# Optimization experiments

Measured on AMD Instinct MI355X. Metric: run time of the kernel, lower is better.

## Reference

```python
import jax, jax.numpy as jnp
import numpy as np

B, L, D, H = 8192, 32, 128, 8  # batch nodes, max neighbors, embed dim, heads


def setup_inputs() -> dict:
    key = jax.random.key(0)
    ks = jax.random.split(key, 16)
    s = 0.05  # weight init scale
    return {
        "node_embeds": jax.random.normal(ks[0], (B, D), jnp.float32),
        "neighbor_embeds": jax.random.normal(ks[1], (B, L, D), jnp.float32),
        "node_degrees": jax.random.randint(ks[2], (B,), 1, L + 1),
        # layer 0 (concatenate=True): query_heads 128->1024, value_proj 128->128
        "wq0": jax.random.normal(ks[3], (H * D, D), jnp.float32) * s,
        "bq0": jax.random.normal(ks[4], (H * D,), jnp.float32) * s,
        "wv0": jax.random.normal(ks[5], (D, D), jnp.float32) * s,
        "bv0": jax.random.normal(ks[6], (D,), jnp.float32) * s,
        "wp0": jax.random.normal(ks[7], (D, D), jnp.float32) * s,
        "bp0": jax.random.normal(ks[8], (D,), jnp.float32) * s,
        # layer 1 (last, concatenate=False): query_heads 128->1024, value_proj 128->1024
        "wq1": jax.random.normal(ks[9], (H * D, D), jnp.float32) * s,
        "bq1": jax.random.normal(ks[10], (H * D,), jnp.float32) * s,
        "wv1": jax.random.normal(ks[11], (H * D, D), jnp.float32) * s,
        "bv1": jax.random.normal(ks[12], (H * D,), jnp.float32) * s,
        "wp1": jax.random.normal(ks[13], (D, D), jnp.float32) * s,
        "bp1": jax.random.normal(ks[14], (D,), jnp.float32) * s,
    }


def _attn_layer(node, neigh, mask, wq, bq, wv, bv, wp, bp, concatenate):
    # neigh: [B, L, D] (already zero-masked); mask: [B, L] bool
    b, l, d = neigh.shape
    dk = d  # attnhead_size == query_size == D for use_dot=True
    v = neigh @ wv.T + bv                      # [B, L, H*dv]
    dv = v.shape[-1] // H
    v = v.reshape(b, l, H, dv).transpose(0, 2, 1, 3)   # [B, H, L, dv]
    q = (node @ wq.T + bq).reshape(b, H, dk)           # [B, H, dk]
    scores = jnp.einsum('bhd,bld->bhl', q, neigh) / jnp.sqrt(jnp.float32(dk))
    scores = jnp.where(mask[:, None, :], scores, jnp.float32(-1e9))
    p = jax.nn.softmax(scores, axis=-1)                # [B, H, L]
    av = jnp.einsum('bhl,bhld->bhd', p, v)             # [B, H, dv]
    av = av.reshape(b, H * dv) if concatenate else av.mean(axis=1)
    return node @ wp.T + bp + av


def reference(node_embeds, neighbor_embeds, node_degrees,
              wq0, bq0, wv0, bv0, wp0, bp0,
              wq1, bq1, wv1, bv1, wp1, bp1):
    mask = jnp.arange(L)[None, :] < node_degrees[:, None]          # [B, L]
    neigh = jnp.where(mask[:, :, None], neighbor_embeds, 0.0)
    x = _attn_layer(node_embeds, neigh, mask, wq0, bq0, wv0, bv0, wp0, bp0, True)
    x = jax.nn.relu(x)  # activation on all but last layer
    x = _attn_layer(x, neigh, mask, wq1, bq1, wv1, bv1, wp1, bp1, False)
    return x
```

## Files before the change

### kernel.cpp

```cpp
#include <hip/hip_runtime.h>

constexpr int Ln = 32, Dn = 128, Hn = 8;

using bf16x8 = __attribute__((ext_vector_type(8))) short;
using f32x4  = __attribute__((ext_vector_type(4))) float;

__device__ __forceinline__ unsigned short f2bf(float f) {
    union { float f; unsigned u; } v; v.f = f;
    unsigned r = v.u + 0x7FFFu + ((v.u >> 16) & 1u);
    return (unsigned short)(r >> 16);
}
__device__ __forceinline__ float bf2f(unsigned short s) {
    union { unsigned u; float f; } v; v.u = ((unsigned)s) << 16; return v.f;
}
__device__ __forceinline__ bf16x8 cvt8(float4 a, float4 b) {
    bf16x8 r;
    r[0] = (short)f2bf(a.x); r[1] = (short)f2bf(a.y);
    r[2] = (short)f2bf(a.z); r[3] = (short)f2bf(a.w);
    r[4] = (short)f2bf(b.x); r[5] = (short)f2bf(b.y);
    r[6] = (short)f2bf(b.z); r[7] = (short)f2bf(b.w);
    return r;
}

constexpr int    CVT_ITEMS = 442368 + 2304;
constexpr size_t WS_NEED   = 442368ull * 2 + 2304ull * 4;

__global__ void cvt_weights(const float* __restrict__ wq0, const float* __restrict__ bq0,
                            const float* __restrict__ wv0, const float* __restrict__ bv0,
                            const float* __restrict__ wp0, const float* __restrict__ bp0,
                            const float* __restrict__ wq1, const float* __restrict__ bq1,
                            const float* __restrict__ wv1, const float* __restrict__ bv1,
                            const float* __restrict__ wp1, const float* __restrict__ bp1,
                            unsigned short* __restrict__ ws)
{
    const float scale = 0.08838834764831845f;
    int tid = blockIdx.x * 256 + threadIdx.x;
    if (tid >= CVT_ITEMS) return;
    if (tid < 442368) {
        float v;
        if      (tid < 131072) v = wq0[tid] * scale;
        else if (tid < 262144) v = wq1[tid - 131072] * scale;
        else if (tid < 278528) v = wv0[tid - 262144];
        else if (tid < 294912) v = wp0[tid - 278528];
        else if (tid < 425984) v = wv1[tid - 294912] * 0.125f;
        else                   v = wp1[tid - 425984];
        ws[tid] = f2bf(v);
    } else {
        int j = tid - 442368;
        float* fws = (float*)(ws + 442368);
        if      (j < 1024) fws[j] = bq0[j] * scale;
        else if (j < 2048) fws[j] = bq1[j - 1024] * scale;
        else if (j < 2176) { int d = j - 2048; fws[j] = bp0[d] + bv0[d]; }
        else if (j < 2304) {
            int d = j - 2176;
            float s = 0.f;
            #pragma unroll
            for (int h = 0; h < Hn; ++h) s += bv1[h * Dn + d];
            fws[j] = bp1[d] + 0.125f * s;
        }
    }
}

__global__ __launch_bounds__(512, 4)
void gcn11(const float* __restrict__ nodeE, const float* __restrict__ neighE,
           const int* __restrict__ degp, const unsigned short* __restrict__ ws,
           float* __restrict__ out)
{
    __shared__ unsigned short sN[8][16][136];
    __shared__ unsigned short sQC[16 * 1096];
    __shared__ unsigned short sX[16][136];
    __shared__ float          sP[8][16][Hn];
    __shared__ float          sSum[8][Hn];
    __shared__ int            sDeg[16];

    const unsigned short* wq0b = ws;
    const unsigned short* wq1b = ws + 131072;
    const unsigned short* wv0b = ws + 262144;
    const unsigned short* wp0b = ws + 278528;
    const unsigned short* wv1b = ws + 294912;
    const unsigned short* wp1b = ws + 425984;
    const float* fws  = (const float*)(ws + 442368);
    const float* bq0s = fws;
    const float* bq1s = fws + 1024;
    const float* b0   = fws + 2048;
    const float* b1   = fws + 2176;

    const int t    = threadIdx.x;
    const int lane = t & 63;
    const int w    = t >> 6;
    const int row  = lane & 15;
    const int kg   = lane >> 4;
    const int node0 = blockIdx.x * 16;

    bf16x8 a[4];

    auto stage_half = [&](int node, int r0, int v) {
        const float* base = neighE + ((size_t)(node0 + node) * Ln + r0) * Dn;
        #pragma unroll
        for (int it = 0; it < 4; ++it) {
            int c = lane + 64 * it;
            int l = c >> 4, d8 = c & 15;
            if (l < v) {
                const float4* s = (const float4*)(base + (size_t)c * 8);
                *(bf16x8*)&sN[w][l][d8 * 8] = cvt8(s[0], s[1]);
            }
        }
    };

    auto qgemm = [&](const unsigned short* wqb, const float* bqs) {
        #pragma unroll
        for (int ks = 0; ks < 4; ++ks)
            a[ks] = *(const bf16x8*)&sX[row][ks * 32 + kg * 8];
        #pragma unroll
        for (int f = 0; f < 8; ++f) {
            int o = w * 128 + f * 16 + row;
            f32x4 acc = {0.f, 0.f, 0.f, 0.f};
            #pragma unroll
            for (int ks = 0; ks < 4; ++ks)
                acc = __builtin_amdgcn_mfma_f32_16x16x32_bf16(
                    a[ks], *(const bf16x8*)(wqb + (size_t)o * Dn + ks * 32 + kg * 8), acc, 0, 0, 0);
            float bias = bqs[o];
            #pragma unroll
            for (int rr = 0; rr < 4; ++rr)
                sQC[(kg * 4 + rr) * 1096 + w * 136 + f * 16 + row] = f2bf(acc[rr] + bias);
        }
    };

    auto pv_acc = [&](float (&c)[Hn][2], int v) {
        for (int l = 0; l < v; ++l) {
            unsigned nv = *(const unsigned*)&sN[w][l][2 * lane];
            float n0 = bf2f((unsigned short)(nv & 0xFFFFu));
            float n1 = bf2f((unsigned short)(nv >> 16));
            float4 p01 = *(const float4*)&sP[w][l][0];
            float4 p23 = *(const float4*)&sP[w][l][4];
            c[0][0] += p01.x * n0; c[0][1] += p01.x * n1;
            c[1][0] += p01.y * n0; c[1][1] += p01.y * n1;
            c[2][0] += p01.z * n0; c[2][1] += p01.z * n1;
            c[3][0] += p01.w * n0; c[3][1] += p01.w * n1;
            c[4][0] += p23.x * n0; c[4][1] += p23.x * n1;
            c[5][0] += p23.y * n0; c[5][1] += p23.y * n1;
            c[6][0] += p23.z * n0; c[6][1] += p23.z * n1;
            c[7][0] += p23.w * n0; c[7][1] += p23.w * n1;
        }
    };

    auto attn2 = [&](int node) {
        const int deg = sDeg[node];
        const int v0  = deg < 16 ? deg : 16;
        stage_half(node, 0, v0);

        const int hcol = row & 7;
        bf16x8 qf[4];
        #pragma unroll
        for (int ks = 0; ks < 4; ++ks)
            qf[ks] = *(const bf16x8*)&sQC[node * 1096 + hcol * 136 + ks * 32 + kg * 8];

        f32x4 s0 = {0.f,0.f,0.f,0.f};
        #pragma unroll
        for (int ks = 0; ks < 4; ++ks)
            s0 = __builtin_amdgcn_mfma_f32_16x16x32_bf16(
                *(const bf16x8*)&sN[w][row][ks * 32 + kg * 8], qf[ks], s0, 0, 0, 0);
        float sv[4];
        float sum = 0.f;
        #pragma unroll
        for (int j = 0; j < 4; ++j) {
            int l = kg * 4 + j;
            sv[j] = (l < v0) ? __expf(s0[j]) : 0.f;
            sum += sv[j];
        }
        sum += __shfl_xor(sum, 16);
        sum += __shfl_xor(sum, 32);
        if (row < 8) {
            #pragma unroll
            for (int j = 0; j < 4; ++j)
                sP[w][kg * 4 + j][row] = sv[j];
        }
        float c[Hn][2];
        #pragma unroll
        for (int h = 0; h < Hn; ++h) { c[h][0] = 0.f; c[h][1] = 0.f; }
        pv_acc(c, v0);

        if (deg > 16) {
            const int v1 = deg - 16;
            stage_half(node, 16, v1);
            f32x4 s1 = {0.f,0.f,0.f,0.f};
            #pragma unroll
            for (int ks = 0; ks < 4; ++ks)
                s1 = __builtin_amdgcn_mfma_f32_16x16x32_bf16(
                    *(const bf16x8*)&sN[w][row][ks * 32 + kg * 8], qf[ks], s1, 0, 0, 0);
            float sw[4];
            float sum1 = 0.f;
            #pragma unroll
            for (int j = 0; j < 4; ++j) {
                int l = kg * 4 + j;
                sw[j] = (l < v1) ? __expf(s1[j]) : 0.f;
                sum1 += sw[j];
            }
            sum1 += __shfl_xor(sum1, 16);
            sum1 += __shfl_xor(sum1, 32);
            sum += sum1;
            if (row < 8) {
                #pragma unroll
                for (int j = 0; j < 4; ++j)
                    sP[w][kg * 4 + j][row] = sw[j];
            }
            pv_acc(c, v1);
        }

        if (row < 8) sSum[w][row] = sum;
        float4 r01 = *(const float4*)&sSum[w][0];
        float4 r23 = *(const float4*)&sSum[w][4];
        float rh[Hn] = {r01.x, r01.y, r01.z, r01.w, r23.x, r23.y, r23.z, r23.w};
        #pragma unroll
        for (int h = 0; h < Hn; ++h) {
            float inv = 1.f / rh[h];
            unsigned pk = (unsigned)f2bf(c[h][0] * inv) | ((unsigned)f2bf(c[h][1] * inv) << 16);
            *(unsigned*)&sQC[node * 1096 + h * 136 + 2 * lane] = pk;
        }
    };

    if (t < 256) {
        int r = t >> 4, c = (t & 15) * 8;
        const float4* s = (const float4*)(nodeE + (size_t)(node0 + r) * Dn + c);
        *(bf16x8*)&sX[r][c] = cvt8(s[0], s[1]);
    }
    if (t < 16) sDeg[t] = degp[node0 + t];
    __syncthreads();

    qgemm(wq0b, bq0s);
    __syncthreads();

    attn2(w);
    attn2(8 + w);
    __syncthreads();

    {
        const int d = w * 16 + row;
        f32x4 pa = {0.f,0.f,0.f,0.f}, va = {0.f,0.f,0.f,0.f};
        #pragma unroll
        for (int ks = 0; ks < 4; ++ks) {
            pa = __builtin_amdgcn_mfma_f32_16x16x32_bf16(
                a[ks], *(const bf16x8*)(wp0b + (size_t)d * Dn + ks * 32 + kg * 8), pa, 0, 0, 0);
            bf16x8 c0 = *(const bf16x8*)&sQC[row * 1096 + w * 136 + ks * 32 + kg * 8];
            va = __builtin_amdgcn_mfma_f32_16x16x32_bf16(
                c0, *(const bf16x8*)(wv0b + (size_t)d * Dn + ks * 32 + kg * 8), va, 0, 0, 0);
        }
        float bias = b0[d];
        #pragma unroll
        for (int rr = 0; rr < 4; ++rr)
            sX[kg * 4 + rr][d] = f2bf(fmaxf(pa[rr] + va[rr] + bias, 0.f));
    }
    __syncthreads();

    qgemm(wq1b, bq1s);
    __syncthreads();

    attn2(w);
    attn2(8 + w);
    __syncthreads();

    {
        const int d = w * 16 + row;
        f32x4 pa = {0.f,0.f,0.f,0.f};
        #pragma unroll
        for (int ks = 0; ks < 4; ++ks)
            pa = __builtin_amdgcn_mfma_f32_16x16x32_bf16(
                a[ks], *(const bf16x8*)(wp1b + (size_t)d * Dn + ks * 32 + kg * 8), pa, 0, 0, 0);
        f32x4 g = {0.f,0.f,0.f,0.f};
        #pragma unroll 8
        for (int ks2 = 0; ks2 < 32; ++ks2) {
            int hk = ks2 * 32 + kg * 8;
            int h = hk >> 7, kk = hk & 127;
            bf16x8 c0 = *(const bf16x8*)&sQC[row * 1096 + h * 136 + kk];
            g = __builtin_amdgcn_mfma_f32_16x16x32_bf16(
                c0, *(const bf16x8*)(wv1b + ((size_t)(h * Dn + d)) * Dn + kk), g, 0, 0, 0);
        }
        float bias = b1[d];
        #pragma unroll
        for (int rr = 0; rr < 4; ++rr)
            out[(size_t)(node0 + kg * 4 + rr) * Dn + d] = pa[rr] + g[rr] + bias;
    }
}

__global__ __launch_bounds__(256, 2)
void gcn2(const float* __restrict__ nodeE, const float* __restrict__ neighE,
          const int* __restrict__ degp,
          const float* __restrict__ wq0, const float* __restrict__ bq0,
          const float* __restrict__ wv0, const float* __restrict__ bv0,
          const float* __restrict__ wp0, const float* __restrict__ bp0,
          const float* __restrict__ wq1, const float* __restrict__ bq1,
          const float* __restrict__ wv1, const float* __restrict__ bv1,
          const float* __restrict__ wp1, const float* __restrict__ bp1,
          float* __restrict__ out)
{
    __shared__ unsigned short sX[16][Dn];
    __shared__ unsigned short sQ[8][Hn][Dn];
    __shared__ unsigned short sN[4][Ln][Dn + 8];
    __shared__ float          sP[4][Hn][Ln];
    __shared__ unsigned short sC[8][Hn][Dn + 8];
    __shared__ int            sDeg[8];

    const int t    = threadIdx.x;
    const int lane = t & 63;
    const int w    = t >> 6;
    const int row  = lane & 15;
    const int kg   = lane >> 4;
    const int node0 = blockIdx.x * 8;
    const float scale = 0.08838834764831845f;

    {
        int i = t * 8, r = i >> 7, c = i & 127;
        if (r < 8) {
            const float4* s = (const float4*)(nodeE + (size_t)(node0 + r) * Dn + c);
            *(bf16x8*)&sX[r][c] = cvt8(s[0], s[1]);
        } else {
            bf16x8 z = {0,0,0,0,0,0,0,0};
            *(bf16x8*)&sX[r][c] = z;
        }
        if (t < 8) sDeg[t] = degp[node0 + t];
    }
    __syncthreads();

    auto qgemm = [&](const float* wq, const float* bq) {
        bf16x8 a[4];
        #pragma unroll
        for (int ks = 0; ks < 4; ++ks)
            a[ks] = *(const bf16x8*)&sX[row][ks*32 + kg*8];
        for (int f = 0; f < 16; ++f) {
            int o = w*256 + f*16 + row;
            f32x4 acc = {0.f, 0.f, 0.f, 0.f};
            #pragma unroll
            for (int ks = 0; ks < 4; ++ks) {
                const float4* wp4 = (const float4*)(wq + (size_t)o*Dn + ks*32 + kg*8);
                acc = __builtin_amdgcn_mfma_f32_16x16x32_bf16(a[ks], cvt8(wp4[0], wp4[1]), acc, 0, 0, 0);
            }
            float bias = bq[o];
            if (kg < 2) {
                #pragma unroll
                for (int rr = 0; rr < 4; ++rr) {
                    int nd = kg*4 + rr;
                    sQ[nd][o >> 7][o & 127] = f2bf((acc[rr] + bias) * scale);
                }
            }
        }
    };

    auto attn = [&](int b) {
        #pragma unroll
        for (int it = 0; it < 8; ++it) {
            int e8 = t + 256 * it;
            int n = e8 >> 9, l = (e8 >> 4) & 31, d8 = e8 & 15;
            const float4* s = (const float4*)(neighE + ((size_t)(node0 + b*4 + n)*Ln + l)*Dn + d8*8);
            *(bf16x8*)&sN[n][l][d8*8] = cvt8(s[0], s[1]);
        }
        __syncthreads();

        const int deg  = sDeg[b*4 + w];
        const int hcol = row & 7;
        bf16x8 qf[4];
        #pragma unroll
        for (int ks = 0; ks < 4; ++ks)
            qf[ks] = *(const bf16x8*)&sQ[b*4 + w][hcol][ks*32 + kg*8];

        f32x4 s0 = {0.f,0.f,0.f,0.f}, s1 = {0.f,0.f,0.f,0.f};
        #pragma unroll
        for (int ks = 0; ks < 4; ++ks) {
            bf16x8 a0 = *(const bf16x8*)&sN[w][row][ks*32 + kg*8];
            bf16x8 a1 = *(const bf16x8*)&sN[w][16 + row][ks*32 + kg*8];
            s0 = __builtin_amdgcn_mfma_f32_16x16x32_bf16(a0, qf[ks], s0, 0, 0, 0);
            s1 = __builtin_amdgcn_mfma_f32_16x16x32_bf16(a1, qf[ks], s1, 0, 0, 0);
        }
        float sv[8];
        #pragma unroll
        for (int rr = 0; rr < 4; ++rr) { sv[rr] = s0[rr]; sv[4+rr] = s1[rr]; }
        float m = -3.0e38f;
        #pragma unroll
        for (int j = 0; j < 8; ++j) {
            int l = (j >> 2)*16 + kg*4 + (j & 3);
            if (l >= deg) sv[j] = -3.0e38f;
            m = fmaxf(m, sv[j]);
        }
        m = fmaxf(m, __shfl_xor(m, 16));
        m = fmaxf(m, __shfl_xor(m, 32));
        float sum = 0.f;
        #pragma unroll
        for (int j = 0; j < 8; ++j) {
            float e = (sv[j] > -1.0e38f) ? __expf(sv[j] - m) : 0.f;
            sv[j] = e; sum += e;
        }
        sum += __shfl_xor(sum, 16);
        sum += __shfl_xor(sum, 32);
        float rinv = 1.f / sum;
        if (row < 8) {
            #pragma unroll
            for (int j = 0; j < 8; ++j) {
                int l = (j >> 2)*16 + kg*4 + (j & 3);
                sP[w][row][l] = sv[j] * rinv;
            }
        }

        float c[Hn][2];
        #pragma unroll
        for (int h = 0; h < Hn; ++h) { c[h][0] = 0.f; c[h][1] = 0.f; }
        #pragma unroll 4
        for (int l = 0; l < Ln; ++l) {
            unsigned nv = *(const unsigned*)&sN[w][l][2*lane];
            float n0 = bf2f((unsigned short)(nv & 0xFFFFu));
            float n1 = bf2f((unsigned short)(nv >> 16));
            #pragma unroll
            for (int h = 0; h < Hn; ++h) {
                float p = sP[w][h][l];
                c[h][0] += p * n0; c[h][1] += p * n1;
            }
        }
        #pragma unroll
        for (int h = 0; h < Hn; ++h) {
            unsigned pk = (unsigned)f2bf(c[h][0]) | ((unsigned)f2bf(c[h][1]) << 16);
            *(unsigned*)&sC[b*4 + w][h][2*lane] = pk;
        }
        __syncthreads();
    };

    auto ep0 = [&]() {
        bf16x8 a1[4];
        #pragma unroll
        for (int ks = 0; ks < 4; ++ks)
            a1[ks] = *(const bf16x8*)&sX[row][ks*32 + kg*8];
        float xn[2][4]; int dd[2];
        #pragma unroll
        for (int fi = 0; fi < 2; ++fi) {
            int f = 2*w + fi;
            int d = f*16 + row; dd[fi] = d;
            f32x4 acc = {0.f,0.f,0.f,0.f}, acc2 = {0.f,0.f,0.f,0.f};
            #pragma unroll
            for (int ks = 0; ks < 4; ++ks) {
                const float4* bp = (const float4*)(wp0 + (size_t)d*Dn + ks*32 + kg*8);
                acc = __builtin_amdgcn_mfma_f32_16x16x32_bf16(a1[ks], cvt8(bp[0], bp[1]), acc, 0, 0, 0);
                bf16x8 a2 = *(const bf16x8*)&sC[row & 7][f][ks*32 + kg*8];
                const float4* vp = (const float4*)(wv0 + (size_t)d*Dn + ks*32 + kg*8);
                acc2 = __builtin_amdgcn_mfma_f32_16x16x32_bf16(a2, cvt8(vp[0], vp[1]), acc2, 0, 0, 0);
            }
            float bias = bp0[d] + bv0[d];
            #pragma unroll
            for (int rr = 0; rr < 4; ++rr)
                xn[fi][rr] = fmaxf(acc[rr] + acc2[rr] + bias, 0.f);
        }
        __syncthreads();
        if (kg < 2) {
            #pragma unroll
            for (int fi = 0; fi < 2; ++fi)
                #pragma unroll
                for (int rr = 0; rr < 4; ++rr)
                    sX[kg*4 + rr][dd[fi]] = f2bf(xn[fi][rr]);
        }
        __syncthreads();
    };

    auto ep1 = [&]() {
        bf16x8 a1[4];
        #pragma unroll
        for (int ks = 0; ks < 4; ++ks)
            a1[ks] = *(const bf16x8*)&sX[row][ks*32 + kg*8];
        #pragma unroll
        for (int fi = 0; fi < 2; ++fi) {
            int f = 2*w + fi;
            int d = f*16 + row;
            f32x4 acc = {0.f,0.f,0.f,0.f};
            #pragma unroll
            for (int ks = 0; ks < 4; ++ks) {
                const float4* bp = (const float4*)(wp1 + (size_t)d*Dn + ks*32 + kg*8);
                acc = __builtin_amdgcn_mfma_f32_16x16x32_bf16(a1[ks], cvt8(bp[0], bp[1]), acc, 0, 0, 0);
            }
            f32x4 acc2 = {0.f,0.f,0.f,0.f};
            for (int ks2 = 0; ks2 < 32; ++ks2) {
                int hk = ks2*32 + kg*8;
                int h = hk >> 7, kk = hk & 127;
                bf16x8 a2 = *(const bf16x8*)&sC[row & 7][h][kk];
                const float4* vp = (const float4*)(wv1 + ((size_t)(h*Dn + d))*Dn + kk);
                acc2 = __builtin_amdgcn_mfma_f32_16x16x32_bf16(a2, cvt8(vp[0], vp[1]), acc2, 0, 0, 0);
            }
            float bsum = 0.f;
            #pragma unroll
            for (int h = 0; h < Hn; ++h) bsum += bv1[h*Dn + d];
            float bias = bp1[d] + 0.125f * bsum;
            if (kg < 2) {
                #pragma unroll
                for (int rr = 0; rr < 4; ++rr) {
                    int nd = kg*4 + rr;
                    out[(size_t)(node0 + nd)*Dn + d] = acc[rr] + 0.125f*acc2[rr] + bias;
                }
            }
        }
    };

    qgemm(wq0, bq0);
    __syncthreads();
    attn(0);
    attn(1);
    ep0();
    qgemm(wq1, bq1);
    __syncthreads();
    attn(0);
    attn(1);
    ep1();
}

extern "C" void kernel_launch(void* const* d_in, const int* in_sizes, int n_in,
                              void* d_out, int out_size, void* d_ws, size_t ws_size,
                              hipStream_t stream) {
    const float* nodeE  = (const float*)d_in[0];
    const float* neighE = (const float*)d_in[1];
    const int*   degp   = (const int*)d_in[2];
    const float* wq0 = (const float*)d_in[3];
    const float* bq0 = (const float*)d_in[4];
    const float* wv0 = (const float*)d_in[5];
    const float* bv0 = (const float*)d_in[6];
    const float* wp0 = (const float*)d_in[7];
    const float* bp0 = (const float*)d_in[8];
    const float* wq1 = (const float*)d_in[9];
    const float* bq1 = (const float*)d_in[10];
    const float* wv1 = (const float*)d_in[11];
    const float* bv1 = (const float*)d_in[12];
    const float* wp1 = (const float*)d_in[13];
    const float* bp1 = (const float*)d_in[14];
    float* outp = (float*)d_out;

    if (ws_size >= WS_NEED) {
        unsigned short* ws = (unsigned short*)d_ws;
        hipLaunchKernelGGL(cvt_weights, dim3((CVT_ITEMS + 255) / 256), dim3(256), 0, stream,
                           wq0, bq0, wv0, bv0, wp0, bp0,
                           wq1, bq1, wv1, bv1, wp1, bp1, ws);
        hipLaunchKernelGGL(gcn11, dim3(512), dim3(512), 0, stream,
                           nodeE, neighE, degp, ws, outp);
    } else {
        hipLaunchKernelGGL(gcn2, dim3(1024), dim3(256), 0, stream,
                           nodeE, neighE, degp,
                           wq0, bq0, wv0, bv0, wp0, bp0,
                           wq1, bq1, wv1, bv1, wp1, bp1, outp);
    }
}
```

Measured before the change: 84.37 us.

## Register-prefetch next neighbor tile to overlap global loads with attention math

Neighbor-embedding loads move into a register prefetch buffer (pf[8] float4) that is issued one stage ahead: the next half-tile or the next node's first half is loaded while the current tile's scores and PV accumulation run. The first tile is prefetched before the qgemm prologue, and in layer 0 the last node prefetches the layer-1 first tile. This hides global-memory latency of the neighbor stream at the cost of 32 extra VGPRs per thread under launch_bounds(512,4), which could raise spill or occupancy pressure.

```diff
diff --git a/kernel.cpp b/kernel.cpp
--- a/kernel.cpp
+++ b/kernel.cpp
@@ -62,7 +62,7 @@
 }
 
 __global__ __launch_bounds__(512, 4)
-void gcn11(const float* __restrict__ nodeE, const float* __restrict__ neighE,
+void gcn12(const float* __restrict__ nodeE, const float* __restrict__ neighE,
            const int* __restrict__ degp, const unsigned short* __restrict__ ws,
            float* __restrict__ out)
 {
@@ -93,17 +93,27 @@
     const int node0 = blockIdx.x * 16;
 
     bf16x8 a[4];
-
-    auto stage_half = [&](int node, int r0, int v) {
+    float4 pf[8];
+
+    auto issue_pf = [&](int node, int r0, int v) {
         const float* base = neighE + ((size_t)(node0 + node) * Ln + r0) * Dn;
+        #pragma unroll
+        for (int it = 0; it < 4; ++it) {
+            int c = lane + 64 * it;
+            if ((c >> 4) < v) {
+                const float4* s = (const float4*)(base + (size_t)c * 8);
+                pf[2 * it]     = s[0];
+                pf[2 * it + 1] = s[1];
+            }
+        }
+    };
+    auto write_pf = [&](int v) {
         #pragma unroll
         for (int it = 0; it < 4; ++it) {
             int c = lane + 64 * it;
             int l = c >> 4, d8 = c & 15;
-            if (l < v) {
-                const float4* s = (const float4*)(base + (size_t)c * 8);
-                *(bf16x8*)&sN[w][l][d8 * 8] = cvt8(s[0], s[1]);
-            }
+            if (l < v)
+                *(bf16x8*)&sN[w][l][d8 * 8] = cvt8(pf[2 * it], pf[2 * it + 1]);
         }
     };
 
@@ -144,10 +154,13 @@
         }
     };
 
-    auto attn2 = [&](int node) {
+    auto attn2 = [&](int node, int nxt) {
         const int deg = sDeg[node];
         const int v0  = deg < 16 ? deg : 16;
-        stage_half(node, 0, v0);
+        write_pf(v0);
+        const bool hasB = deg > 16;
+        if (hasB)          issue_pf(node, 16, deg - 16);
+        else if (nxt >= 0) issue_pf(nxt, 0, sDeg[nxt] < 16 ? sDeg[nxt] : 16);
 
         const int hcol = row & 7;
         bf16x8 qf[4];
@@ -180,9 +193,10 @@
         for (int h = 0; h < Hn; ++h) { c[h][0] = 0.f; c[h][1] = 0.f; }
         pv_acc(c, v0);
 
-        if (deg > 16) {
+        if (hasB) {
             const int v1 = deg - 16;
-            stage_half(node, 16, v1);
+            write_pf(v1);
+            if (nxt >= 0) issue_pf(nxt, 0, sDeg[nxt] < 16 ? sDeg[nxt] : 16);
             f32x4 s1 = {0.f,0.f,0.f,0.f};
             #pragma unroll
             for (int ks = 0; ks < 4; ++ks)
@@ -219,6 +233,10 @@
         }
     };
 
+    {
+        int dw = degp[node0 + w];
+        issue_pf(w, 0, dw < 16 ? dw : 16);
+    }
     if (t < 256) {
         int r = t >> 4, c = (t & 15) * 8;
         const float4* s = (const float4*)(nodeE + (size_t)(node0 + r) * Dn + c);
@@ -230,8 +248,8 @@
     qgemm(wq0b, bq0s);
     __syncthreads();
 
-    attn2(w);
-    attn2(8 + w);
+    attn2(w, 8 + w);
+    attn2(8 + w, w);
     __syncthreads();
 
     {
@@ -255,8 +273,8 @@
     qgemm(wq1b, bq1s);
     __syncthreads();
 
-    attn2(w);
-    attn2(8 + w);
+    attn2(w, 8 + w);
+    attn2(8 + w, -1);
     __syncthreads();
 
     {
@@ -530,7 +548,7 @@
         hipLaunchKernelGGL(cvt_weights, dim3((CVT_ITEMS + 255) / 256), dim3(256), 0, stream,
                            wq0, bq0, wv0, bv0, wp0, bp0,
                            wq1, bq1, wv1, bv1, wp1, bp1, ws);
-        hipLaunchKernelGGL(gcn11, dim3(512), dim3(512), 0, stream,
+        hipLaunchKernelGGL(gcn12, dim3(512), dim3(512), 0, stream,
                            nodeE, neighE, degp, ws, outp);
     } else {
         hipLaunchKernelGGL(gcn2, dim3(1024), dim3(256), 0, stream,
```

Result: slower. 102.4 us (+21.3%).
